# Kernel optimization log

Hardware: AMD Instinct MI355X
Metric: run time of the kernel (lower is better)

## Reference

```python
import jax, jax.numpy as jnp
import numpy as np

T, B, I, H, L = 512, 64, 512, 1024, 2


def setup_inputs() -> dict:
    key = jax.random.key(0)
    ks = jax.random.split(key, 11)
    s = 0.03  # keep tanh recurrence in a sane range
    return {
        "x": jax.random.normal(ks[0], (T, B, I), jnp.float32),
        "hidden": jnp.zeros((L, B, H), jnp.float32),
        "W_ih0": jax.random.normal(ks[1], (H, I), jnp.float32) * s,
        "W_hh0": jax.random.normal(ks[2], (H, H), jnp.float32) * s,
        "b_ih0": jax.random.normal(ks[3], (H,), jnp.float32) * s,
        "b_hh0": jax.random.normal(ks[4], (H,), jnp.float32) * s,
        "W_ih1": jax.random.normal(ks[5], (H, H), jnp.float32) * s,
        "W_hh1": jax.random.normal(ks[6], (H, H), jnp.float32) * s,
        "b_ih1": jax.random.normal(ks[7], (H,), jnp.float32) * s,
        "b_hh1": jax.random.normal(ks[8], (H,), jnp.float32) * s,
        "W_fc": jax.random.normal(ks[9], (I, H), jnp.float32) * s,
        "b_fc": jax.random.normal(ks[10], (I,), jnp.float32) * s,
    }


def _rnn_layer(x_proj, h0, W_hh, b_hh):
    # x_proj: [T, B, H] = x @ W_ih.T + b_ih, precomputed as one big GEMM.
    # h_t = tanh(x_proj_t + h_{t-1} @ W_hh.T + b_hh)
    def step(h, xp):
        h_new = jnp.tanh(xp + h @ W_hh.T + b_hh)
        return h_new, h_new
    _, ys = jax.lax.scan(step, h0, x_proj)
    return ys  # [T, B, H]


def reference(x, hidden, W_ih0, W_hh0, b_ih0, b_hh0,
              W_ih1, W_hh1, b_ih1, b_hh1, W_fc, b_fc):
    # Layer 0 (input -> hidden), then layer 1 (hidden -> hidden), tanh RNN.
    out0 = _rnn_layer(jnp.einsum("tbi,hi->tbh", x, W_ih0) + b_ih0,
                      hidden[0], W_hh0, b_hh0)
    out1 = _rnn_layer(jnp.einsum("tbh,gh->tbg", out0, W_ih1) + b_ih1,
                      hidden[1], W_hh1, b_hh1)
    # Trailing Linear(hidden_dim_rnn -> input_size) applied per timestep.
    return jnp.einsum("tbh,ih->tbi", out1, W_fc) + b_fc
```

## Files before the change

kernel.cpp:

```cpp
#include <hip/hip_runtime.h>
#include <stdint.h>

#define T_DIM 512
#define B_DIM 64
#define I_DIM 512
#define H_DIM 1024
#define BH ((size_t)B_DIM * H_DIM)

typedef __attribute__((ext_vector_type(8))) short short8;
typedef __attribute__((ext_vector_type(4))) float f32x4;

__device__ __forceinline__ unsigned short f2bf(float f) {
    unsigned int u = __float_as_uint(f);
    unsigned int r = (u + 0x7FFFu + ((u >> 16) & 1u)) >> 16;
    return (unsigned short)r;
}
__device__ __forceinline__ float bf2f(unsigned short b) {
    return __uint_as_float(((unsigned int)b) << 16);
}
__device__ __forceinline__ float fast_tanh(float x) {
    x = fminf(fmaxf(x, -15.f), 15.f);
    float e = __expf(2.f * x);
    return (e - 1.f) / (e + 1.f);
}

__device__ __forceinline__ void wait_group(const int* flags) {
    if (threadIdx.x < 64) {
        while (__hip_atomic_load(&flags[threadIdx.x], __ATOMIC_RELAXED,
                                 __HIP_MEMORY_SCOPE_AGENT) == 0)
            __builtin_amdgcn_s_sleep(2);
        __threadfence();
    }
    __syncthreads();
}
__device__ __forceinline__ void signal_flag(int* flag) {
    __syncthreads();
    if (threadIdx.x == 0) {
        __threadfence();
        __hip_atomic_store(flag, 1, __ATOMIC_RELAXED, __HIP_MEMORY_SCOPE_AGENT);
    }
}

__global__ void conv_f2bf(const float* __restrict__ in, unsigned short* __restrict__ out, int n4) {
    int i = blockIdx.x * blockDim.x + threadIdx.x;
    int stride = gridDim.x * blockDim.x;
    for (int idx = i; idx < n4; idx += stride) {
        float4 v = reinterpret_cast<const float4*>(in)[idx];
        ushort4 o;
        o.x = f2bf(v.x); o.y = f2bf(v.y); o.z = f2bf(v.z); o.w = f2bf(v.w);
        reinterpret_cast<ushort4*>(out)[idx] = o;
    }
}

__global__ void bias_sum(const float* __restrict__ a, const float* __restrict__ b,
                         float* __restrict__ o, int n) {
    int i = blockIdx.x * blockDim.x + threadIdx.x;
    if (i < n) o[i] = a[i] + b[i];
}

template <int OUT_BF16>
__global__ void gemm_bias(const unsigned short* __restrict__ A,
                          const unsigned short* __restrict__ W,
                          const float* __restrict__ bias,
                          void* __restrict__ Cout,
                          int M, int N, int K) {
    const int ntn = N >> 6;
    const int mt = blockIdx.x / ntn;
    const int nt = blockIdx.x % ntn;
    const int m_base = mt << 6, n_base = nt << 6;
    const int lane = threadIdx.x & 63;
    const int wave = threadIdx.x >> 6;
    const int wm = wave >> 1, wn = wave & 1;
    const int r0 = lane & 15;
    const int g  = lane >> 4;
    const int koff = g << 3;

    f32x4 acc[2][2];
    for (int i = 0; i < 2; i++)
        for (int j = 0; j < 2; j++)
            acc[i][j] = (f32x4)(0.f);

    const unsigned short* Arow0 = A + (size_t)(m_base + wm * 32 + r0) * K + koff;
    const unsigned short* Wrow0 = W + (size_t)(n_base + wn * 32 + r0) * K + koff;

    for (int k0 = 0; k0 < K; k0 += 32) {
        short8 a0 = *reinterpret_cast<const short8*>(Arow0 + k0);
        short8 a1 = *reinterpret_cast<const short8*>(Arow0 + (size_t)16 * K + k0);
        short8 b0 = *reinterpret_cast<const short8*>(Wrow0 + k0);
        short8 b1 = *reinterpret_cast<const short8*>(Wrow0 + (size_t)16 * K + k0);
        acc[0][0] = __builtin_amdgcn_mfma_f32_16x16x32_bf16(a0, b0, acc[0][0], 0, 0, 0);
        acc[0][1] = __builtin_amdgcn_mfma_f32_16x16x32_bf16(a0, b1, acc[0][1], 0, 0, 0);
        acc[1][0] = __builtin_amdgcn_mfma_f32_16x16x32_bf16(a1, b0, acc[1][0], 0, 0, 0);
        acc[1][1] = __builtin_amdgcn_mfma_f32_16x16x32_bf16(a1, b1, acc[1][1], 0, 0, 0);
    }

    for (int mi = 0; mi < 2; mi++) {
        for (int ni = 0; ni < 2; ni++) {
            for (int r = 0; r < 4; r++) {
                int row = m_base + wm * 32 + mi * 16 + g * 4 + r;
                int col = n_base + wn * 32 + ni * 16 + r0;
                float v = acc[mi][ni][r] + bias[col];
                if (OUT_BF16)
                    ((unsigned short*)Cout)[(size_t)row * N + col] = f2bf(v);
                else
                    ((float*)Cout)[(size_t)row * N + col] = v;
            }
        }
    }
}

__global__ void __launch_bounds__(256, 1)
rnn_persist(const unsigned short* __restrict__ xp0,
            const unsigned short* __restrict__ whh0,
            const unsigned short* __restrict__ wih1,
            const unsigned short* __restrict__ whh1,
            const float* __restrict__ bias1,
            const unsigned short* __restrict__ hinit,
            unsigned short* __restrict__ out0,
            unsigned short* __restrict__ out1,
            int* __restrict__ flags0,
            int* __restrict__ flags1)
{
    extern __shared__ char smem[];
    const int lane = threadIdx.x & 63;
    const int wave = threadIdx.x >> 6;
    const int r0 = lane & 15;
    const int g = lane >> 4;
    const int koff = g << 3;
    const int wg = blockIdx.x;
    const int brow = (wave << 4) + r0;

    if (wg < 64) {
        const int n0 = wg << 4;
        for (int i = threadIdx.x; i < 2048; i += 256) {
            const int c = i >> 7, kc = i & 127;
            short8 v = *reinterpret_cast<const short8*>(
                whh0 + (size_t)(n0 + c) * H_DIM + (kc << 3));
            *reinterpret_cast<short8*>(smem + ((((kc << 4) + c)) << 4)) = v;
        }
        __syncthreads();
        const int col = n0 + r0;
        const char* Bp = smem + (g << 8) + (r0 << 4);

        for (int t = 0; t < T_DIM; ++t) {
            if (t) wait_group(flags0 + (size_t)(t - 1) * 64);
            const unsigned short* hp = t ? out0 + (size_t)(t - 1) * BH : hinit;
            const unsigned short* Ap = hp + (size_t)brow * H_DIM + koff;
            f32x4 acc[4];
            acc[0] = acc[1] = acc[2] = acc[3] = (f32x4)(0.f);
            short8 ar[16];
            #pragma unroll
            for (int h = 0; h < 2; ++h) {
                #pragma unroll
                for (int i = 0; i < 16; ++i)
                    ar[i] = *reinterpret_cast<const short8*>(Ap + (h << 9) + (i << 5));
                #pragma unroll
                for (int i = 0; i < 16; ++i) {
                    short8 b = *reinterpret_cast<const short8*>(
                        Bp + (size_t)((h << 4) + i) * 1024);
                    acc[i & 3] = __builtin_amdgcn_mfma_f32_16x16x32_bf16(ar[i], b, acc[i & 3], 0, 0, 0);
                }
            }
            f32x4 s = acc[0] + acc[1] + acc[2] + acc[3];
            const unsigned short* xp = xp0 + (size_t)t * BH;
            unsigned short* o = out0 + (size_t)t * BH;
            #pragma unroll
            for (int r = 0; r < 4; ++r) {
                const int row = (wave << 4) + (g << 2) + r;
                float v = fast_tanh(s[r] + bf2f(xp[(size_t)row * H_DIM + col]));
                o[(size_t)row * H_DIM + col] = f2bf(v);
            }
            signal_flag(&flags0[(size_t)t * 64 + wg]);
        }
    } else {
        const int wg2 = wg - 64;
        const int n0 = wg2 << 4;
        for (int i = threadIdx.x; i < 4096; i += 256) {
            const int c = i >> 8, kc = i & 255;
            const unsigned short* src = (kc < 128)
                ? wih1 + (size_t)(n0 + c) * H_DIM + (kc << 3)
                : whh1 + (size_t)(n0 + c) * H_DIM + ((kc - 128) << 3);
            short8 v = *reinterpret_cast<const short8*>(src);
            *reinterpret_cast<short8*>(smem + ((((kc << 4) + c)) << 4)) = v;
        }
        __syncthreads();
        const int col = n0 + r0;
        const float b1 = bias1[col];
        const char* Bp = smem + (g << 8) + (r0 << 4);

        for (int t = 0; t < T_DIM; ++t) {
            wait_group(flags0 + (size_t)t * 64);
            if (t) wait_group(flags1 + (size_t)(t - 1) * 64);
            const unsigned short* a0 = out0 + (size_t)t * BH;
            const unsigned short* h1 = t ? out1 + (size_t)(t - 1) * BH : hinit + BH;
            f32x4 acc[4];
            acc[0] = acc[1] = acc[2] = acc[3] = (f32x4)(0.f);
            short8 ar[16];
            #pragma unroll
            for (int h = 0; h < 4; ++h) {
                const unsigned short* Ap = ((h < 2) ? a0 : h1)
                    + (size_t)brow * H_DIM + koff + ((size_t)(h & 1) << 9);
                #pragma unroll
                for (int i = 0; i < 16; ++i)
                    ar[i] = *reinterpret_cast<const short8*>(Ap + (i << 5));
                #pragma unroll
                for (int i = 0; i < 16; ++i) {
                    short8 b = *reinterpret_cast<const short8*>(
                        Bp + (size_t)((h << 4) + i) * 1024);
                    acc[i & 3] = __builtin_amdgcn_mfma_f32_16x16x32_bf16(ar[i], b, acc[i & 3], 0, 0, 0);
                }
            }
            f32x4 s = acc[0] + acc[1] + acc[2] + acc[3];
            unsigned short* o = out1 + (size_t)t * BH;
            #pragma unroll
            for (int r = 0; r < 4; ++r) {
                const int row = (wave << 4) + (g << 2) + r;
                float v = fast_tanh(s[r] + b1);
                o[(size_t)row * H_DIM + col] = f2bf(v);
            }
            signal_flag(&flags1[(size_t)t * 64 + wg2]);
        }
    }
}

extern "C" void kernel_launch(void* const* d_in, const int* in_sizes, int n_in,
                              void* d_out, int out_size, void* d_ws, size_t ws_size,
                              hipStream_t stream) {
    const float* x      = (const float*)d_in[0];
    const float* hidden = (const float*)d_in[1];
    const float* W_ih0  = (const float*)d_in[2];
    const float* W_hh0  = (const float*)d_in[3];
    const float* b_ih0  = (const float*)d_in[4];
    const float* b_hh0  = (const float*)d_in[5];
    const float* W_ih1  = (const float*)d_in[6];
    const float* W_hh1  = (const float*)d_in[7];
    const float* b_ih1  = (const float*)d_in[8];
    const float* b_hh1  = (const float*)d_in[9];
    const float* W_fc   = (const float*)d_in[10];
    const float* b_fc   = (const float*)d_in[11];

    char* ws = (char*)d_ws;
    size_t off = 0;
    auto alloc = [&](size_t bytes) -> char* {
        char* p = ws + off;
        off += (bytes + 255) & ~(size_t)255;
        return p;
    };
    const size_t TBH = (size_t)T_DIM * B_DIM * H_DIM;
    const size_t TBI = (size_t)T_DIM * B_DIM * I_DIM;

    unsigned short* xb     = (unsigned short*)alloc(TBI * 2);
    unsigned short* wih0b  = (unsigned short*)alloc((size_t)H_DIM * I_DIM * 2);
    unsigned short* whh0b  = (unsigned short*)alloc((size_t)H_DIM * H_DIM * 2);
    unsigned short* wih1b  = (unsigned short*)alloc((size_t)H_DIM * H_DIM * 2);
    unsigned short* whh1b  = (unsigned short*)alloc((size_t)H_DIM * H_DIM * 2);
    unsigned short* wfcb   = (unsigned short*)alloc((size_t)I_DIM * H_DIM * 2);
    unsigned short* hinitb = (unsigned short*)alloc((size_t)2 * B_DIM * H_DIM * 2);
    float* bias0 = (float*)alloc(H_DIM * 4);
    float* bias1 = (float*)alloc(H_DIM * 4);
    unsigned short* xp0    = (unsigned short*)alloc(TBH * 2);
    unsigned short* out0b  = (unsigned short*)alloc(TBH * 2);
    unsigned short* out1b  = (unsigned short*)alloc(TBH * 2);
    int* flags0 = (int*)alloc((size_t)T_DIM * 64 * 4);
    int* flags1 = (int*)alloc((size_t)T_DIM * 64 * 4);

    auto conv = [&](const float* in, unsigned short* out, int n) {
        int n4 = n / 4;
        int blocks = (n4 + 255) / 256;
        if (blocks > 2048) blocks = 2048;
        conv_f2bf<<<blocks, 256, 0, stream>>>(in, out, n4);
    };
    conv(x, xb, (int)TBI);
    conv(W_ih0, wih0b, H_DIM * I_DIM);
    conv(W_hh0, whh0b, H_DIM * H_DIM);
    conv(W_ih1, wih1b, H_DIM * H_DIM);
    conv(W_hh1, whh1b, H_DIM * H_DIM);
    conv(W_fc, wfcb, I_DIM * H_DIM);
    conv(hidden, hinitb, 2 * B_DIM * H_DIM);
    bias_sum<<<4, 256, 0, stream>>>(b_ih0, b_hh0, bias0, H_DIM);
    bias_sum<<<4, 256, 0, stream>>>(b_ih1, b_hh1, bias1, H_DIM);

    (void)hipMemsetAsync(flags0, 0, (size_t)T_DIM * 64 * 4 * 2, stream);

    {
        int M = T_DIM * B_DIM, N = H_DIM, K = I_DIM;
        dim3 grid((M / 64) * (N / 64));
        gemm_bias<1><<<grid, 256, 0, stream>>>(xb, wih0b, bias0, xp0, M, N, K);
    }

    {
        void* args[] = {(void*)&xp0, (void*)&whh0b, (void*)&wih1b, (void*)&whh1b,
                        (void*)&bias1, (void*)&hinitb, (void*)&out0b, (void*)&out1b,
                        (void*)&flags0, (void*)&flags1};
        (void)hipLaunchCooperativeKernel(reinterpret_cast<void*>(rnn_persist),
                                         dim3(128), dim3(256), args, 65536, stream);
    }

    {
        int M = T_DIM * B_DIM, N = I_DIM, K = H_DIM;
        dim3 grid((M / 64) * (N / 64));
        gemm_bias<0><<<grid, 256, 0, stream>>>(out1b, wfcb, b_fc, d_out, M, N, K);
    }
}
```

Baseline: 7.922 ms.

## Halve persistent RNN workgroups, widen column tiles, use relaxed atomic loads instead of fences

The persistent RNN kernel now runs 32+32 workgroups, each owning 32 hidden columns, instead of 64+64 with 16 columns, so each step waits on fewer flags. Hidden-state loads and stores become agent-scope relaxed atomic 64-bit accesses, and the thread fences around flag signalling are removed. Results are transposed through LDS so each lane writes 8 contiguous bf16 values. The intent is to cut per-timestep synchronisation latency and improve store coalescing. The cost is half as many CUs doing the per-step GEMM, a large static LDS allocation, and weaker memory ordering that relies on the atomic accesses for visibility.

```diff
diff --git a/kernel.cpp b/kernel.cpp
--- a/kernel.cpp
+++ b/kernel.cpp
@@ -6,6 +6,8 @@
 #define I_DIM 512
 #define H_DIM 1024
 #define BH ((size_t)B_DIM * H_DIM)
+#define NW0 32
+#define NW1 32
 
 typedef __attribute__((ext_vector_type(8))) short short8;
 typedef __attribute__((ext_vector_type(4))) float f32x4;
@@ -24,21 +26,23 @@
     return (e - 1.f) / (e + 1.f);
 }
 
-__device__ __forceinline__ void wait_group(const int* flags) {
-    if (threadIdx.x < 64) {
-        while (__hip_atomic_load(&flags[threadIdx.x], __ATOMIC_RELAXED,
-                                 __HIP_MEMORY_SCOPE_AGENT) == 0)
-            __builtin_amdgcn_s_sleep(2);
-        __threadfence();
-    }
-    __syncthreads();
-}
-__device__ __forceinline__ void signal_flag(int* flag) {
-    __syncthreads();
-    if (threadIdx.x == 0) {
-        __threadfence();
-        __hip_atomic_store(flag, 1, __ATOMIC_RELAXED, __HIP_MEMORY_SCOPE_AGENT);
-    }
+__device__ __forceinline__ unsigned long long ld64_sys(const unsigned short* p) {
+    return __hip_atomic_load((const unsigned long long*)p, __ATOMIC_RELAXED,
+                             __HIP_MEMORY_SCOPE_AGENT);
+}
+__device__ __forceinline__ short8 ldA_sys(const unsigned short* p) {
+    union { unsigned long long u[2]; short8 v; } t;
+    t.u[0] = ld64_sys(p);
+    t.u[1] = ld64_sys(p + 4);
+    return t.v;
+}
+__device__ __forceinline__ void st64_sys(unsigned short* p, unsigned long long v) {
+    __hip_atomic_store((unsigned long long*)p, v, __ATOMIC_RELAXED,
+                       __HIP_MEMORY_SCOPE_AGENT);
+}
+__device__ __forceinline__ void spin1(const int* f) {
+    while (__hip_atomic_load(f, __ATOMIC_RELAXED, __HIP_MEMORY_SCOPE_AGENT) == 0)
+        __builtin_amdgcn_s_sleep(1);
 }
 
 __global__ void conv_f2bf(const float* __restrict__ in, unsigned short* __restrict__ out, int n4) {
@@ -121,104 +125,168 @@
             int* __restrict__ flags0,
             int* __restrict__ flags1)
 {
-    extern __shared__ char smem[];
-    const int lane = threadIdx.x & 63;
-    const int wave = threadIdx.x >> 6;
+    __shared__ __attribute__((aligned(16))) char smem[140288];
+    const int tid  = threadIdx.x;
+    const int lane = tid & 63;
+    const int wave = tid >> 6;
     const int r0 = lane & 15;
-    const int g = lane >> 4;
-    const int koff = g << 3;
+    const int g  = lane >> 4;
     const int wg = blockIdx.x;
     const int brow = (wave << 4) + r0;
 
-    if (wg < 64) {
-        const int n0 = wg << 4;
-        for (int i = threadIdx.x; i < 2048; i += 256) {
-            const int c = i >> 7, kc = i & 127;
-            short8 v = *reinterpret_cast<const short8*>(
-                whh0 + (size_t)(n0 + c) * H_DIM + (kc << 3));
-            *reinterpret_cast<short8*>(smem + ((((kc << 4) + c)) << 4)) = v;
+    const char* Bp = smem + (g << 9) + (r0 << 4);
+    float* sc = (float*)(smem + 131072) + wave * 576;
+    const int rr = lane >> 2;
+    const int cc = (lane & 3) << 3;
+    const int orow = (wave << 4) + rr;
+
+    if (wg < NW0) {
+        const int n0 = wg << 5;
+        for (int i = tid; i < 4096; i += 256) {
+            const int c = i & 31, kc = i >> 5;
+            *reinterpret_cast<short8*>(smem + (((kc << 5) + c) << 4)) =
+                *reinterpret_cast<const short8*>(whh0 + (size_t)(n0 + c) * H_DIM + (kc << 3));
         }
         __syncthreads();
-        const int col = n0 + r0;
-        const char* Bp = smem + (g << 8) + (r0 << 4);
+        const int gcol = n0 + cc;
 
         for (int t = 0; t < T_DIM; ++t) {
-            if (t) wait_group(flags0 + (size_t)(t - 1) * 64);
+            if (t) {
+                if (tid < 32) spin1(&flags0[(size_t)(t - 1) * 32 + tid]);
+                __syncthreads();
+            }
             const unsigned short* hp = t ? out0 + (size_t)(t - 1) * BH : hinit;
-            const unsigned short* Ap = hp + (size_t)brow * H_DIM + koff;
-            f32x4 acc[4];
-            acc[0] = acc[1] = acc[2] = acc[3] = (f32x4)(0.f);
+            const unsigned short* Ap = hp + (size_t)brow * H_DIM + (g << 3);
+            f32x4 acc[2][4];
+            #pragma unroll
+            for (int a = 0; a < 2; ++a)
+                #pragma unroll
+                for (int b = 0; b < 4; ++b) acc[a][b] = (f32x4)(0.f);
             short8 ar[16];
             #pragma unroll
             for (int h = 0; h < 2; ++h) {
                 #pragma unroll
                 for (int i = 0; i < 16; ++i)
-                    ar[i] = *reinterpret_cast<const short8*>(Ap + (h << 9) + (i << 5));
+                    ar[i] = ldA_sys(Ap + ((h * 16 + i) << 5));
                 #pragma unroll
                 for (int i = 0; i < 16; ++i) {
-                    short8 b = *reinterpret_cast<const short8*>(
-                        Bp + (size_t)((h << 4) + i) * 1024);
-                    acc[i & 3] = __builtin_amdgcn_mfma_f32_16x16x32_bf16(ar[i], b, acc[i & 3], 0, 0, 0);
+                    const char* bp = Bp + (size_t)(h * 16 + i) * 2048;
+                    short8 b0 = *reinterpret_cast<const short8*>(bp);
+                    short8 b1 = *reinterpret_cast<const short8*>(bp + 256);
+                    acc[0][i & 3] = __builtin_amdgcn_mfma_f32_16x16x32_bf16(ar[i], b0, acc[0][i & 3], 0, 0, 0);
+                    acc[1][i & 3] = __builtin_amdgcn_mfma_f32_16x16x32_bf16(ar[i], b1, acc[1][i & 3], 0, 0, 0);
                 }
             }
-            f32x4 s = acc[0] + acc[1] + acc[2] + acc[3];
-            const unsigned short* xp = xp0 + (size_t)t * BH;
-            unsigned short* o = out0 + (size_t)t * BH;
+            f32x4 s0 = (acc[0][0] + acc[0][1]) + (acc[0][2] + acc[0][3]);
+            f32x4 s1 = (acc[1][0] + acc[1][1]) + (acc[1][2] + acc[1][3]);
             #pragma unroll
             for (int r = 0; r < 4; ++r) {
-                const int row = (wave << 4) + (g << 2) + r;
-                float v = fast_tanh(s[r] + bf2f(xp[(size_t)row * H_DIM + col]));
-                o[(size_t)row * H_DIM + col] = f2bf(v);
-            }
-            signal_flag(&flags0[(size_t)t * 64 + wg]);
+                sc[(g * 4 + r) * 36 + r0]      = s0[r];
+                sc[(g * 4 + r) * 36 + 16 + r0] = s1[r];
+            }
+            __builtin_amdgcn_sched_barrier(0);
+            f32x4 t0 = *reinterpret_cast<const f32x4*>(sc + rr * 36 + cc);
+            f32x4 t1 = *reinterpret_cast<const f32x4*>(sc + rr * 36 + cc + 4);
+            short8 xv = *reinterpret_cast<const short8*>(
+                xp0 + (size_t)t * BH + (size_t)orow * H_DIM + gcol);
+            float v[8];
+            #pragma unroll
+            for (int j = 0; j < 4; ++j) {
+                v[j]     = fast_tanh(t0[j] + bf2f((unsigned short)xv[j]));
+                v[4 + j] = fast_tanh(t1[j] + bf2f((unsigned short)xv[4 + j]));
+            }
+            unsigned long long lo = (unsigned long long)f2bf(v[0])
+                | ((unsigned long long)f2bf(v[1]) << 16)
+                | ((unsigned long long)f2bf(v[2]) << 32)
+                | ((unsigned long long)f2bf(v[3]) << 48);
+            unsigned long long hi = (unsigned long long)f2bf(v[4])
+                | ((unsigned long long)f2bf(v[5]) << 16)
+                | ((unsigned long long)f2bf(v[6]) << 32)
+                | ((unsigned long long)f2bf(v[7]) << 48);
+            unsigned short* o = out0 + (size_t)t * BH + (size_t)orow * H_DIM + gcol;
+            st64_sys(o, lo);
+            st64_sys(o + 4, hi);
+            __syncthreads();
+            if (tid == 0)
+                __hip_atomic_store(&flags0[(size_t)t * 32 + wg], 1,
+                                   __ATOMIC_RELAXED, __HIP_MEMORY_SCOPE_AGENT);
         }
     } else {
-        const int wg2 = wg - 64;
-        const int n0 = wg2 << 4;
-        for (int i = threadIdx.x; i < 4096; i += 256) {
-            const int c = i >> 8, kc = i & 255;
+        const int wg2 = wg - NW0;
+        const int n0 = wg2 << 5;
+        for (int i = tid; i < 8192; i += 256) {
+            const int c = i & 31, kc = i >> 5;
             const unsigned short* src = (kc < 128)
                 ? wih1 + (size_t)(n0 + c) * H_DIM + (kc << 3)
                 : whh1 + (size_t)(n0 + c) * H_DIM + ((kc - 128) << 3);
-            short8 v = *reinterpret_cast<const short8*>(src);
-            *reinterpret_cast<short8*>(smem + ((((kc << 4) + c)) << 4)) = v;
+            *reinterpret_cast<short8*>(smem + (((kc << 5) + c) << 4)) =
+                *reinterpret_cast<const short8*>(src);
         }
         __syncthreads();
-        const int col = n0 + r0;
-        const float b1 = bias1[col];
-        const char* Bp = smem + (g << 8) + (r0 << 4);
+        const int gcol = n0 + cc;
+        const float4 bv0 = *reinterpret_cast<const float4*>(bias1 + gcol);
+        const float4 bv1 = *reinterpret_cast<const float4*>(bias1 + gcol + 4);
 
         for (int t = 0; t < T_DIM; ++t) {
-            wait_group(flags0 + (size_t)t * 64);
-            if (t) wait_group(flags1 + (size_t)(t - 1) * 64);
+            if (tid < 32) spin1(&flags0[(size_t)t * 32 + tid]);
+            else if (t && tid < 64) spin1(&flags1[(size_t)(t - 1) * 32 + (tid - 32)]);
+            __syncthreads();
             const unsigned short* a0 = out0 + (size_t)t * BH;
             const unsigned short* h1 = t ? out1 + (size_t)(t - 1) * BH : hinit + BH;
-            f32x4 acc[4];
-            acc[0] = acc[1] = acc[2] = acc[3] = (f32x4)(0.f);
+            const unsigned short* ApA = a0 + (size_t)brow * H_DIM + (g << 3);
+            const unsigned short* ApH = h1 + (size_t)brow * H_DIM + (g << 3);
+            f32x4 acc[2][4];
+            #pragma unroll
+            for (int a = 0; a < 2; ++a)
+                #pragma unroll
+                for (int b = 0; b < 4; ++b) acc[a][b] = (f32x4)(0.f);
             short8 ar[16];
             #pragma unroll
             for (int h = 0; h < 4; ++h) {
-                const unsigned short* Ap = ((h < 2) ? a0 : h1)
-                    + (size_t)brow * H_DIM + koff + ((size_t)(h & 1) << 9);
+                const unsigned short* Ap = (h < 2) ? ApA : ApH;
+                const int base = (h & 1) << 4;
                 #pragma unroll
                 for (int i = 0; i < 16; ++i)
-                    ar[i] = *reinterpret_cast<const short8*>(Ap + (i << 5));
+                    ar[i] = ldA_sys(Ap + ((base + i) << 5));
                 #pragma unroll
                 for (int i = 0; i < 16; ++i) {
-                    short8 b = *reinterpret_cast<const short8*>(
-                        Bp + (size_t)((h << 4) + i) * 1024);
-                    acc[i & 3] = __builtin_amdgcn_mfma_f32_16x16x32_bf16(ar[i], b, acc[i & 3], 0, 0, 0);
+                    const char* bp = Bp + (size_t)(h * 16 + i) * 2048;
+                    short8 b0 = *reinterpret_cast<const short8*>(bp);
+                    short8 b1 = *reinterpret_cast<const short8*>(bp + 256);
+                    acc[0][i & 3] = __builtin_amdgcn_mfma_f32_16x16x32_bf16(ar[i], b0, acc[0][i & 3], 0, 0, 0);
+                    acc[1][i & 3] = __builtin_amdgcn_mfma_f32_16x16x32_bf16(ar[i], b1, acc[1][i & 3], 0, 0, 0);
                 }
             }
-            f32x4 s = acc[0] + acc[1] + acc[2] + acc[3];
-            unsigned short* o = out1 + (size_t)t * BH;
+            f32x4 s0 = (acc[0][0] + acc[0][1]) + (acc[0][2] + acc[0][3]);
+            f32x4 s1 = (acc[1][0] + acc[1][1]) + (acc[1][2] + acc[1][3]);
             #pragma unroll
             for (int r = 0; r < 4; ++r) {
-                const int row = (wave << 4) + (g << 2) + r;
-                float v = fast_tanh(s[r] + b1);
-                o[(size_t)row * H_DIM + col] = f2bf(v);
-            }
-            signal_flag(&flags1[(size_t)t * 64 + wg2]);
+                sc[(g * 4 + r) * 36 + r0]      = s0[r];
+                sc[(g * 4 + r) * 36 + 16 + r0] = s1[r];
+            }
+            __builtin_amdgcn_sched_barrier(0);
+            f32x4 t0 = *reinterpret_cast<const f32x4*>(sc + rr * 36 + cc);
+            f32x4 t1 = *reinterpret_cast<const f32x4*>(sc + rr * 36 + cc + 4);
+            float v[8];
+            v[0] = fast_tanh(t0[0] + bv0.x); v[1] = fast_tanh(t0[1] + bv0.y);
+            v[2] = fast_tanh(t0[2] + bv0.z); v[3] = fast_tanh(t0[3] + bv0.w);
+            v[4] = fast_tanh(t1[0] + bv1.x); v[5] = fast_tanh(t1[1] + bv1.y);
+            v[6] = fast_tanh(t1[2] + bv1.z); v[7] = fast_tanh(t1[3] + bv1.w);
+            unsigned long long lo = (unsigned long long)f2bf(v[0])
+                | ((unsigned long long)f2bf(v[1]) << 16)
+                | ((unsigned long long)f2bf(v[2]) << 32)
+                | ((unsigned long long)f2bf(v[3]) << 48);
+            unsigned long long hi = (unsigned long long)f2bf(v[4])
+                | ((unsigned long long)f2bf(v[5]) << 16)
+                | ((unsigned long long)f2bf(v[6]) << 32)
+                | ((unsigned long long)f2bf(v[7]) << 48);
+            unsigned short* o = out1 + (size_t)t * BH + (size_t)orow * H_DIM + gcol;
+            st64_sys(o, lo);
+            st64_sys(o + 4, hi);
+            __syncthreads();
+            if (tid == 0)
+                __hip_atomic_store(&flags1[(size_t)t * 32 + wg2], 1,
+                                   __ATOMIC_RELAXED, __HIP_MEMORY_SCOPE_AGENT);
         }
     }
 }
@@ -261,8 +329,8 @@
     unsigned short* xp0    = (unsigned short*)alloc(TBH * 2);
     unsigned short* out0b  = (unsigned short*)alloc(TBH * 2);
     unsigned short* out1b  = (unsigned short*)alloc(TBH * 2);
-    int* flags0 = (int*)alloc((size_t)T_DIM * 64 * 4);
-    int* flags1 = (int*)alloc((size_t)T_DIM * 64 * 4);
+    int* flags0 = (int*)alloc((size_t)T_DIM * 32 * 4);
+    int* flags1 = (int*)alloc((size_t)T_DIM * 32 * 4);
 
     auto conv = [&](const float* in, unsigned short* out, int n) {
         int n4 = n / 4;
@@ -274,13 +342,13 @@
     conv(W_ih0, wih0b, H_DIM * I_DIM);
     conv(W_hh0, whh0b, H_DIM * H_DIM);
     conv(W_ih1, wih1b, H_DIM * H_DIM);
-    conv(W_hh1, whh1b, H_DIM * H_DIM);
     conv(W_fc, wfcb, I_DIM * H_DIM);
     conv(hidden, hinitb, 2 * B_DIM * H_DIM);
+    conv(W_hh1, whh1b, H_DIM * H_DIM);
     bias_sum<<<4, 256, 0, stream>>>(b_ih0, b_hh0, bias0, H_DIM);
     bias_sum<<<4, 256, 0, stream>>>(b_ih1, b_hh1, bias1, H_DIM);
 
-    (void)hipMemsetAsync(flags0, 0, (size_t)T_DIM * 64 * 4 * 2, stream);
+    (void)hipMemsetAsync(flags0, 0, (size_t)T_DIM * 32 * 4 * 2, stream);
 
     {
         int M = T_DIM * B_DIM, N = H_DIM, K = I_DIM;
@@ -293,7 +361,7 @@
                         (void*)&bias1, (void*)&hinitb, (void*)&out0b, (void*)&out1b,
                         (void*)&flags0, (void*)&flags1};
         (void)hipLaunchCooperativeKernel(reinterpret_cast<void*>(rnn_persist),
-                                         dim3(128), dim3(256), args, 65536, stream);
+                                         dim3(NW0 + NW1), dim3(256), args, 0, stream);
     }
 
     {
```

Result: slower. 8.748 ms (+10.4%).
